# Performance work log

Hardware: AMD Instinct MI355X
Metric: run time of the kernel (lower is better)

Reference implementation:

```python
import jax, jax.numpy as jnp
import numpy as np

N_NODES = 50000
N_GRAPHS = 32
NODE_F = 16
GLOBAL_F = 2
HID = 300
LAT = 100
N_EDGES = 800000


def _glorot(key, shape):
    fan_in, fan_out = shape[0], shape[1]
    s = jnp.sqrt(2.0 / (fan_in + fan_out))
    return jax.random.normal(key, shape, dtype=jnp.float32) * s


def setup_inputs() -> dict:
    key = jax.random.key(0)
    ks = jax.random.split(key, 24)
    x = jax.random.normal(ks[0], (N_NODES, NODE_F), dtype=jnp.float32)
    edge_index = jax.random.randint(ks[1], (2, N_EDGES), 0, N_NODES, dtype=jnp.int64)
    batch = jnp.sort(jax.random.randint(ks[2], (N_NODES,), 0, N_GRAPHS, dtype=jnp.int64))
    u = jax.random.normal(ks[3], (N_GRAPHS, GLOBAL_F), dtype=jnp.float32)
    # layer 0: in=NODE_F, layer 1: in=LAT
    p = {}
    p['l0_w1'] = _glorot(ks[4], (2 * NODE_F, HID)); p['l0_b1'] = jnp.zeros((HID,), jnp.float32)
    p['l0_w2'] = _glorot(ks[5], (HID, HID));        p['l0_b2'] = jnp.zeros((HID,), jnp.float32)
    p['l0_w3'] = _glorot(ks[6], (HID, LAT));        p['l0_b3'] = jnp.zeros((LAT,), jnp.float32)
    p['l1_w1'] = _glorot(ks[7], (2 * LAT, HID));    p['l1_b1'] = jnp.zeros((HID,), jnp.float32)
    p['l1_w2'] = _glorot(ks[8], (HID, HID));        p['l1_b2'] = jnp.zeros((HID,), jnp.float32)
    p['l1_w3'] = _glorot(ks[9], (HID, LAT));        p['l1_b3'] = jnp.zeros((LAT,), jnp.float32)
    p['lin_w1'] = _glorot(ks[10], (LAT + GLOBAL_F, LAT)); p['lin_b1'] = jnp.zeros((LAT,), jnp.float32)
    p['lin_w2'] = _glorot(ks[11], (LAT, LAT));            p['lin_b2'] = jnp.zeros((LAT,), jnp.float32)
    p['lin_w3'] = _glorot(ks[12], (LAT, 1));              p['lin_b3'] = jnp.zeros((1,), jnp.float32)
    return dict(x=x, edge_index=edge_index, batch=batch, u=u, **p)


def _edge_layer(x, src, dst, w1, b1, w2, b2, w3, b3):
    # gather endpoints; torch_geometric default flow: x_j = x[src], x_i = x[dst]
    xi = x[dst]
    xj = x[src]
    inp = jnp.concatenate([xi, xj - xi], axis=-1)          # [E, 2*in]
    h = jax.nn.relu(inp @ w1 + b1)
    h = jax.nn.relu(h @ w2 + b2)
    m = h @ w3 + b3                                         # [E, out]
    s = jax.ops.segment_sum(m, dst, num_segments=N_NODES)  # scatter-sum to target nodes
    cnt = jax.ops.segment_sum(jnp.ones((m.shape[0],), m.dtype), dst, num_segments=N_NODES)
    return s / jnp.maximum(cnt, 1.0)[:, None]               # scatter-mean


def _mean_pool(x, batch):
    s = jax.ops.segment_sum(x, batch, num_segments=N_GRAPHS)
    cnt = jax.ops.segment_sum(jnp.ones((x.shape[0],), x.dtype), batch, num_segments=N_GRAPHS)
    return s / jnp.maximum(cnt, 1.0)[:, None]


def reference(x, edge_index, batch, u,
              l0_w1, l0_b1, l0_w2, l0_b2, l0_w3, l0_b3,
              l1_w1, l1_b1, l1_w2, l1_b2, l1_w3, l1_b3,
              lin_w1, lin_b1, lin_w2, lin_b2, lin_w3, lin_b3):
    src, dst = edge_index[0], edge_index[1]
    x = _edge_layer(x, src, dst, l0_w1, l0_b1, l0_w2, l0_b2, l0_w3, l0_b3)
    x = jax.nn.relu(x)
    x = _edge_layer(x, src, dst, l1_w1, l1_b1, l1_w2, l1_b2, l1_w3, l1_b3)
    x = jax.nn.relu(x)
    pooled = jnp.concatenate([_mean_pool(x, batch), u], axis=1)  # [G, LAT+GLOBAL_F]
    h = jax.nn.relu(pooled @ lin_w1 + lin_b1)
    h = jax.nn.relu(h @ lin_w2 + lin_b2)
    return h @ lin_w3 + lin_b3  # [G, 1]
```

## Files before the change

kernel.cpp:

```cpp
#include <hip/hip_runtime.h>
#include <cstdint>
#include <cstddef>

#define N_NODES  50000
#define N_GRAPHS 32
#define NODE_F   16
#define GLOBAL_F 2
#define HID      300
#define LAT      100
#define N_EDGES  800000

#define HIDP 320
#define LATP 128
#define NCT1 (HIDP/16)
#define NCT2 (LATP/16)
#define NKS  (HIDP/32)
#define EPB  96
#define NRT  6
#define ROWP 98
#define HSFS 132

typedef __bf16 bf16x8 __attribute__((ext_vector_type(8)));
typedef float  f32x4  __attribute__((ext_vector_type(4)));

__device__ __forceinline__ float relu_f(float x){ return fmaxf(x, 0.f); }

__device__ __forceinline__ unsigned short f2bf(float x){
  unsigned int u = __float_as_uint(x);
  u = (u + 0x7FFFu + ((u >> 16) & 1u)) >> 16;
  return (unsigned short)u;
}
__device__ __forceinline__ unsigned short f2bf_hw(float x){
  __bf16 h = (__bf16)x;
  return __builtin_bit_cast(unsigned short, h);
}
__device__ __forceinline__ float bf2f(unsigned int h){
  return __uint_as_float(h << 16);
}

__global__ void zero_kernel(float* __restrict__ p, int n){
  int i = blockIdx.x*blockDim.x + threadIdx.x;
  if (i < n) p[i] = 0.f;
}

__global__ void hist_kernel(const int* __restrict__ ei, int* __restrict__ hist){
  int e = blockIdx.x*blockDim.x + threadIdx.x;
  if (e < N_EDGES) atomicAdd(&hist[ei[N_EDGES + e]], 1);
}

__global__ __launch_bounds__(256) void scan_kernel(const int* __restrict__ hist,
                                                   int* __restrict__ woff){
  __shared__ int part[256];
  const int t = threadIdx.x;
  const int CH = (N_NODES + 255) / 256;
  const int lo = t*CH, hi = (lo + CH < N_NODES) ? lo + CH : N_NODES;
  int s = 0;
  for (int i = lo; i < hi; ++i) s += hist[i];
  part[t] = s;
  __syncthreads();
  for (int d = 1; d < 256; d <<= 1){
    int v = (t >= d) ? part[t-d] : 0;
    __syncthreads();
    part[t] += v;
    __syncthreads();
  }
  int run = (t == 0) ? 0 : part[t-1];
  for (int i = lo; i < hi; ++i){ woff[i] = run; run += hist[i]; }
}

__global__ void sort_kernel(const int* __restrict__ ei, int* __restrict__ woff,
                            int* __restrict__ es, int* __restrict__ ed){
  int e = blockIdx.x*blockDim.x + threadIdx.x;
  if (e < N_EDGES){
    int s = ei[e], d = ei[N_EDGES + e];
    int pos = atomicAdd(&woff[d], 1);
    es[pos] = s; ed[pos] = d;
  }
}

__global__ void gstart_kernel(const int* __restrict__ batch, int* __restrict__ gstart){
  int n = blockIdx.x*blockDim.x + threadIdx.x;
  if (n < N_NODES){
    int b = batch[n];
    if (n == 0){ for (int g = 0; g <= b; ++g) gstart[g] = 0; }
    else {
      int bp = batch[n-1];
      for (int g = bp+1; g <= b; ++g) gstart[g] = n;
    }
    if (n == N_NODES-1){ for (int g = b+1; g <= N_GRAPHS; ++g) gstart[g] = N_NODES; }
  }
}

__device__ __forceinline__ void pack_one(const float* __restrict__ w, int K, int N,
                                         int nct, unsigned short* __restrict__ out, int i){
  int j  = i & 7;
  int l  = (i >> 3) & 63;
  int t  = i >> 9;
  int ct = t % nct, ks = t / nct;
  int n = ct*16 + (l & 15);
  int k = ks*32 + ((l >> 4) << 3) + j;
  float v = (k < K && n < N) ? w[(size_t)k*N + n] : 0.f;
  out[i] = f2bf(v);
}

#define W2F_ELEMS (NKS*NCT1*512)
#define W3F_ELEMS (NKS*NCT2*512)

__global__ void pack_all(const float* __restrict__ w2a, const float* __restrict__ w3a,
                         const float* __restrict__ w2b, const float* __restrict__ w3b,
                         unsigned short* __restrict__ o2a, unsigned short* __restrict__ o3a,
                         unsigned short* __restrict__ o2b, unsigned short* __restrict__ o3b){
  int i = blockIdx.x*blockDim.x + threadIdx.x;
  if (i < W2F_ELEMS) pack_one(w2a, HID, HID, NCT1, o2a, i);
  else if (i < W2F_ELEMS + W3F_ELEMS) pack_one(w3a, HID, LAT, NCT2, o3a, i - W2F_ELEMS);
  else if (i < 2*W2F_ELEMS + W3F_ELEMS) pack_one(w2b, HID, HID, NCT1, o2b, i - W2F_ELEMS - W3F_ELEMS);
  else if (i < 2*W2F_ELEMS + 2*W3F_ELEMS) pack_one(w3b, HID, LAT, NCT2, o3b, i - 2*W2F_ELEMS - W3F_ELEMS);
}

template<int F>
__global__ void pack_w1frag(const float* __restrict__ w1,
                            unsigned short* __restrict__ out, int total){
  int i = blockIdx.x*blockDim.x + threadIdx.x;
  if (i >= total) return;
  int j  = i & 7;
  int l  = (i >> 3) & 63;
  int t  = i >> 9;
  int ct = t % 40, ks = t / 40;
  int n = ct*16 + (l & 15);
  int k = ks*32 + ((l >> 4) << 3) + j;
  float v = 0.f;
  if (k < F){
    if (n < HIDP){ if (n < HID) v = w1[(size_t)k*HID + n] - w1[(size_t)(F+k)*HID + n]; }
    else { int nn = n - HIDP; if (nn < HID) v = w1[(size_t)(F+k)*HID + nn]; }
  }
  out[i] = f2bf(v);
}

__global__ void pad_bias4(const float* __restrict__ a0, const float* __restrict__ a1,
                          const float* __restrict__ a2, const float* __restrict__ a3,
                          float* __restrict__ o0, float* __restrict__ o1,
                          float* __restrict__ o2, float* __restrict__ o3){
  int i = blockIdx.x*blockDim.x + threadIdx.x;
  if (i < HIDP){
    o0[i] = (i < HID) ? a0[i] : 0.f;
    o1[i] = (i < HID) ? a1[i] : 0.f;
    o2[i] = (i < HID) ? a2[i] : 0.f;
    o3[i] = (i < HID) ? a3[i] : 0.f;
  }
}

__global__ void cvt_x0(const float* __restrict__ x, unsigned short* __restrict__ xb){
  int i = blockIdx.x*blockDim.x + threadIdx.x;
  if (i < N_NODES*32){
    int n = i >> 5, c = i & 31;
    xb[i] = (c < NODE_F) ? f2bf(x[(size_t)n*NODE_F + c]) : 0;
  }
}

template<int KPAD>
__global__ __launch_bounds__(256) void node_gemm(
    const unsigned short* __restrict__ xb, const unsigned short* __restrict__ wf,
    unsigned short* __restrict__ Ub, unsigned short* __restrict__ Vb){
  constexpr int NCH = KPAD/8;
  __shared__ __align__(16) unsigned short at[NCH][66][8];
  const int tid = threadIdx.x;
  const int n0 = blockIdx.x*64;
  for (int i = tid; i < 64*NCH; i += 256){
    int row = i / NCH, c = i % NCH;
    int n = n0 + row; if (n >= N_NODES) n = N_NODES-1;
    *(uint4*)&at[c][row][0] = *(const uint4*)&xb[(size_t)n*KPAD + c*8];
  }
  __syncthreads();
  const int wave = tid >> 6, l = tid & 63;
  const int lrow = l & 15, lq = l >> 4;
  f32x4 acc[4][10];
  #pragma unroll
  for (int rt = 0; rt < 4; ++rt)
    #pragma unroll
    for (int c = 0; c < 10; ++c)
      acc[rt][c] = (f32x4){0.f,0.f,0.f,0.f};
  for (int ks = 0; ks < KPAD/32; ++ks){
    bf16x8 a[4];
    #pragma unroll
    for (int rt = 0; rt < 4; ++rt)
      a[rt] = __builtin_bit_cast(bf16x8, *(const uint4*)&at[4*ks + lq][16*rt + lrow][0]);
    #pragma unroll
    for (int c = 0; c < 10; ++c){
      int ct = wave*10 + c;
      bf16x8 b = __builtin_bit_cast(bf16x8,
                   *(const uint4*)&wf[(((size_t)(ks*40 + ct)) << 9) + l*8]);
      #pragma unroll
      for (int rt = 0; rt < 4; ++rt)
        acc[rt][c] = __builtin_amdgcn_mfma_f32_16x16x32_bf16(a[rt], b, acc[rt][c], 0, 0, 0);
    }
  }
  #pragma unroll
  for (int c = 0; c < 10; ++c){
    int col = (wave*10 + c)*16 + lrow;
    #pragma unroll
    for (int rt = 0; rt < 4; ++rt){
      #pragma unroll
      for (int r = 0; r < 4; ++r){
        int n = n0 + rt*16 + lq*4 + r;
        if (n < N_NODES){
          unsigned short hv = f2bf_hw(acc[rt][c][r]);
          if (col < HIDP) Ub[(size_t)n*HIDP + col] = hv;
          else            Vb[(size_t)n*HIDP + col - HIDP] = hv;
        }
      }
    }
  }
}

__global__ __launch_bounds__(256, 2) void edge_mfma(
    const int* __restrict__ es, const int* __restrict__ ed,
    const unsigned short* __restrict__ U, const unsigned short* __restrict__ V,
    const float* __restrict__ b1p, const unsigned short* __restrict__ w2f,
    const float* __restrict__ b2p, const unsigned short* __restrict__ w3f,
    float* __restrict__ nodeacc){
  __shared__ __align__(16) unsigned char smem[(HIDP/8)*ROWP*8*2];
  __shared__ int sdst[EPB];
  __shared__ int sflag[EPB];
  unsigned short* hsb = (unsigned short*)smem;
  float*          hsf = (float*)smem;
  #define HS(c,row) (hsb + (((c)*ROWP + (row)) << 3))

  const int tid = threadIdx.x;
  const int e0 = blockIdx.x * EPB;
  const int nvalid = (N_EDGES - e0 < EPB) ? (N_EDGES - e0) : EPB;
  if (tid < EPB) sdst[tid] = (tid < nvalid) ? ed[e0 + tid] : -1;

  #pragma unroll
  for (int it = 0; it < 15; ++it){
    int idx = tid + it*256;
    int e = idx / 40;
    int c = idx - e*40;
    int eg = e0 + e; if (eg >= N_EDGES) eg = N_EDGES - 1;
    const int dn = ed[eg], sn = es[eg];
    const uint4 uu = *(const uint4*)&U[(size_t)dn*HIDP + c*8];
    const uint4 vv = *(const uint4*)&V[(size_t)sn*HIDP + c*8];
    const float4 bl = *(const float4*)&b1p[c*8];
    const float4 bh = *(const float4*)&b1p[c*8 + 4];
    const unsigned int uarr[4] = {uu.x, uu.y, uu.z, uu.w};
    const unsigned int varr[4] = {vv.x, vv.y, vv.z, vv.w};
    const float barr[8] = {bl.x, bl.y, bl.z, bl.w, bh.x, bh.y, bh.z, bh.w};
    unsigned int ou[4];
    #pragma unroll
    for (int q = 0; q < 4; ++q){
      float f0 = relu_f(bf2f(uarr[q] & 0xFFFFu) + bf2f(varr[q] & 0xFFFFu) + barr[2*q]);
      float f1 = relu_f(bf2f(uarr[q] >> 16)     + bf2f(varr[q] >> 16)     + barr[2*q+1]);
      ou[q] = (unsigned int)f2bf_hw(f0) | ((unsigned int)f2bf_hw(f1) << 16);
    }
    *(uint4*)HS(c, e) = make_uint4(ou[0], ou[1], ou[2], ou[3]);
  }
  __syncthreads();

  const int wave = tid >> 6, l = tid & 63;
  const int lrow = l & 15, lq = l >> 4;

  f32x4 acc1[NRT][5];
  #pragma unroll
  for (int rt = 0; rt < NRT; ++rt)
    #pragma unroll
    for (int c = 0; c < 5; ++c)
      acc1[rt][c] = (f32x4){0.f,0.f,0.f,0.f};
  for (int ks = 0; ks < NKS; ++ks){
    bf16x8 a[NRT];
    #pragma unroll
    for (int rt = 0; rt < NRT; ++rt)
      a[rt] = __builtin_bit_cast(bf16x8, *(const uint4*)HS(4*ks + lq, 16*rt + lrow));
    #pragma unroll
    for (int c = 0; c < 5; ++c){
      int ct = wave*5 + c;
      bf16x8 b = __builtin_bit_cast(bf16x8,
                   *(const uint4*)&w2f[(((size_t)(ks*NCT1 + ct)) << 9) + l*8]);
      #pragma unroll
      for (int rt = 0; rt < NRT; ++rt)
        acc1[rt][c] = __builtin_amdgcn_mfma_f32_16x16x32_bf16(a[rt], b, acc1[rt][c], 0, 0, 0);
    }
  }
  __syncthreads();

  #pragma unroll
  for (int c = 0; c < 5; ++c){
    int col = (wave*5 + c)*16 + lrow;
    float b2v = b2p[col];
    #pragma unroll
    for (int rt = 0; rt < NRT; ++rt){
      #pragma unroll
      for (int r = 0; r < 4; ++r){
        int row = rt*16 + lq*4 + r;
        HS(col >> 3, row)[col & 7] = f2bf_hw(relu_f(acc1[rt][c][r] + b2v));
      }
    }
  }
  __syncthreads();

  f32x4 acc2[NRT][2];
  #pragma unroll
  for (int rt = 0; rt < NRT; ++rt)
    #pragma unroll
    for (int c = 0; c < 2; ++c)
      acc2[rt][c] = (f32x4){0.f,0.f,0.f,0.f};
  for (int ks = 0; ks < NKS; ++ks){
    bf16x8 a[NRT];
    #pragma unroll
    for (int rt = 0; rt < NRT; ++rt)
      a[rt] = __builtin_bit_cast(bf16x8, *(const uint4*)HS(4*ks + lq, 16*rt + lrow));
    #pragma unroll
    for (int c = 0; c < 2; ++c){
      int ct = wave*2 + c;
      bf16x8 b = __builtin_bit_cast(bf16x8,
                   *(const uint4*)&w3f[(((size_t)(ks*NCT2 + ct)) << 9) + l*8]);
      #pragma unroll
      for (int rt = 0; rt < NRT; ++rt)
        acc2[rt][c] = __builtin_amdgcn_mfma_f32_16x16x32_bf16(a[rt], b, acc2[rt][c], 0, 0, 0);
    }
  }
  __syncthreads();

  #pragma unroll
  for (int c = 0; c < 2; ++c){
    int col = (wave*2 + c)*16 + lrow;
    #pragma unroll
    for (int rt = 0; rt < NRT; ++rt){
      #pragma unroll
      for (int r = 0; r < 4; ++r){
        int row = rt*16 + lq*4 + r;
        hsf[row*HSFS + col] = acc2[rt][c][r];
      }
    }
  }
  if (tid < EPB) sflag[tid] = (tid == 0) || (sdst[tid] != sdst[tid-1]);
  __syncthreads();

  {
    const int col = tid & 127;
    if (col < LAT){
      for (int s = tid >> 7; s < EPB; s += 2){
        if (!sflag[s]) continue;
        int d = sdst[s];
        if (d < 0) continue;
        float sum = hsf[s*HSFS + col];
        int r = s + 1;
        while (r < EPB && !sflag[r]){ sum += hsf[r*HSFS + col]; ++r; }
        atomicAdd(&nodeacc[(size_t)d*LAT + col], sum);
      }
    }
  }
  #undef HS
}

__global__ void finalize_kernel(float* __restrict__ nodeacc, const int* __restrict__ hist,
                                const float* __restrict__ b3,
                                unsigned short* __restrict__ x1b){
  int idx = blockIdx.x*blockDim.x + threadIdx.x;
  if (idx < N_NODES*128){
    int n = idx >> 7, j = idx & 127;
    unsigned short o = 0;
    if (j < LAT){
      int c = hist[n];
      float v = nodeacc[(size_t)n*LAT + j] / fmaxf((float)c, 1.f);
      v += (c > 0) ? b3[j] : 0.f;
      o = f2bf_hw(relu_f(v));
      nodeacc[(size_t)n*LAT + j] = 0.f;
    }
    x1b[idx] = o;
  }
}

__global__ __launch_bounds__(512) void pool_seg(const unsigned short* __restrict__ x1b,
                                                const int* __restrict__ gstart,
                                                float* __restrict__ pooled){
  __shared__ float buf[3][128];
  const int g = blockIdx.x;
  const int lo = gstart[g], hi = gstart[g+1];
  const int col = threadIdx.x & 127, q = threadIdx.x >> 7;
  float s = 0.f;
  for (int n = lo + q; n < hi; n += 4) s += bf2f(x1b[(size_t)n*128 + col]);
  if (q) buf[q-1][col] = s;
  __syncthreads();
  if (q == 0 && col < LAT){
    float tot = s + buf[0][col] + buf[1][col] + buf[2][col];
    pooled[g*LAT + col] = tot / fmaxf((float)(hi - lo), 1.f);
  }
}

__global__ __launch_bounds__(128) void head_kernel(
    const float* __restrict__ pooled,
    const float* __restrict__ u,
    const float* __restrict__ w1, const float* __restrict__ bb1,
    const float* __restrict__ w2, const float* __restrict__ bb2,
    const float* __restrict__ w3, const float* __restrict__ bb3,
    float* __restrict__ out){
  __shared__ float p[N_GRAPHS][LAT+GLOBAL_F];
  __shared__ float h1[N_GRAPHS][LAT];
  __shared__ float h2[N_GRAPHS][LAT];
  const int tid = threadIdx.x;
  for (int t = tid; t < N_GRAPHS*LAT; t += 128){
    int g = t / LAT, k = t - g*LAT;
    p[g][k] = pooled[t];
  }
  for (int t = tid; t < N_GRAPHS*GLOBAL_F; t += 128){
    int g = t / GLOBAL_F, c = t - g*GLOBAL_F;
    p[g][LAT + c] = u[t];
  }
  __syncthreads();
  for (int t = tid; t < N_GRAPHS*LAT; t += 128){
    int g = t / LAT, j = t - g*LAT;
    float s = bb1[j];
    for (int k = 0; k < LAT+GLOBAL_F; k++) s += p[g][k]*w1[(size_t)k*LAT + j];
    h1[g][j] = relu_f(s);
  }
  __syncthreads();
  for (int t = tid; t < N_GRAPHS*LAT; t += 128){
    int g = t / LAT, j = t - g*LAT;
    float s = bb2[j];
    for (int k = 0; k < LAT; k++) s += h1[g][k]*w2[(size_t)k*LAT + j];
    h2[g][j] = relu_f(s);
  }
  __syncthreads();
  for (int t = tid; t < N_GRAPHS; t += 128){
    float s = bb3[0];
    for (int k = 0; k < LAT; k++) s += h2[t][k]*w3[k];
    out[t] = s;
  }
}

extern "C" void kernel_launch(void* const* d_in, const int* in_sizes, int n_in,
                              void* d_out, int out_size, void* d_ws, size_t ws_size,
                              hipStream_t stream){
  (void)in_sizes; (void)n_in; (void)out_size; (void)ws_size;
  const float* x     = (const float*)d_in[0];
  const int*   ei    = (const int*)d_in[1];
  const int*   batch = (const int*)d_in[2];
  const float* u     = (const float*)d_in[3];
  const float* l0_w1 = (const float*)d_in[4];  const float* l0_b1 = (const float*)d_in[5];
  const float* l0_w2 = (const float*)d_in[6];  const float* l0_b2 = (const float*)d_in[7];
  const float* l0_w3 = (const float*)d_in[8];  const float* l0_b3 = (const float*)d_in[9];
  const float* l1_w1 = (const float*)d_in[10]; const float* l1_b1 = (const float*)d_in[11];
  const float* l1_w2 = (const float*)d_in[12]; const float* l1_b2 = (const float*)d_in[13];
  const float* l1_w3 = (const float*)d_in[14]; const float* l1_b3 = (const float*)d_in[15];
  const float* lin_w1= (const float*)d_in[16]; const float* lin_b1= (const float*)d_in[17];
  const float* lin_w2= (const float*)d_in[18]; const float* lin_b2= (const float*)d_in[19];
  const float* lin_w3= (const float*)d_in[20]; const float* lin_b3= (const float*)d_in[21];

  char* wsb = (char*)d_ws;
  const size_t UV_BYTES  = (size_t)N_NODES*HIDP*sizeof(unsigned short);
  const size_t W1F0_ELEMS = (size_t)1*40*512;
  const size_t W1F1_ELEMS = (size_t)4*40*512;

  unsigned short* Ub   = (unsigned short*)wsb;  wsb += UV_BYTES;
  unsigned short* Vb   = (unsigned short*)wsb;  wsb += UV_BYTES;
  unsigned short* w2f0 = (unsigned short*)wsb;  wsb += (size_t)W2F_ELEMS*2;
  unsigned short* w3f0 = (unsigned short*)wsb;  wsb += (size_t)W3F_ELEMS*2;
  unsigned short* w2f1 = (unsigned short*)wsb;  wsb += (size_t)W2F_ELEMS*2;
  unsigned short* w3f1 = (unsigned short*)wsb;  wsb += (size_t)W3F_ELEMS*2;
  unsigned short* w1f0 = (unsigned short*)wsb;  wsb += W1F0_ELEMS*2;
  unsigned short* w1f1 = (unsigned short*)wsb;  wsb += W1F1_ELEMS*2;
  float* b1p0 = (float*)wsb;                    wsb += HIDP*4;
  float* b2p0 = (float*)wsb;                    wsb += HIDP*4;
  float* b1p1 = (float*)wsb;                    wsb += HIDP*4;
  float* b2p1 = (float*)wsb;                    wsb += HIDP*4;
  unsigned short* xb0 = (unsigned short*)wsb;   wsb += (size_t)N_NODES*32*2;
  unsigned short* x1b = (unsigned short*)wsb;   wsb += (size_t)N_NODES*128*2;
  float* nodeacc = (float*)wsb;                 wsb += (size_t)N_NODES*LAT*4;
  int*   hist    = (int*)wsb;                   wsb += (size_t)N_NODES*4;
  int*   woff    = (int*)wsb;                   wsb += (size_t)N_NODES*4;
  int*   es      = (int*)wsb;                   wsb += (size_t)N_EDGES*4;
  int*   ed      = (int*)wsb;                   wsb += (size_t)N_EDGES*4;
  int*   gstart  = (int*)wsb;                   wsb += 64*4;
  float* pooled  = (float*)wsb;                 wsb += (size_t)N_GRAPHS*LAT*4;

  {
    int zn = N_NODES*LAT + N_NODES;
    hipLaunchKernelGGL(zero_kernel, dim3((zn+255)/256), dim3(256), 0, stream, nodeacc, zn);
  }
  hipLaunchKernelGGL(hist_kernel, dim3((N_EDGES+255)/256), dim3(256), 0, stream, ei, hist);
  hipLaunchKernelGGL(scan_kernel, dim3(1), dim3(256), 0, stream, hist, woff);
  hipLaunchKernelGGL(sort_kernel, dim3((N_EDGES+255)/256), dim3(256), 0, stream,
                     ei, woff, es, ed);
  hipLaunchKernelGGL(gstart_kernel, dim3((N_NODES+255)/256), dim3(256), 0, stream,
                     batch, gstart);

  {
    int total = 2*W2F_ELEMS + 2*W3F_ELEMS;
    hipLaunchKernelGGL(pack_all, dim3((total+255)/256), dim3(256), 0, stream,
                       l0_w2, l0_w3, l1_w2, l1_w3, w2f0, w3f0, w2f1, w3f1);
  }
  hipLaunchKernelGGL(pack_w1frag<NODE_F>, dim3(((int)W1F0_ELEMS+255)/256), dim3(256), 0, stream,
                     l0_w1, w1f0, (int)W1F0_ELEMS);
  hipLaunchKernelGGL(pack_w1frag<LAT>, dim3(((int)W1F1_ELEMS+255)/256), dim3(256), 0, stream,
                     l1_w1, w1f1, (int)W1F1_ELEMS);
  hipLaunchKernelGGL(pad_bias4, dim3(2), dim3(256), 0, stream,
                     l0_b1, l0_b2, l1_b1, l1_b2, b1p0, b2p0, b1p1, b2p1);
  hipLaunchKernelGGL(cvt_x0, dim3((N_NODES*32+255)/256), dim3(256), 0, stream, x, xb0);

  const int NGB = (N_NODES + 63)/64;
  const int NEB = (N_EDGES + EPB - 1)/EPB;

  hipLaunchKernelGGL(node_gemm<32>, dim3(NGB), dim3(256), 0, stream, xb0, w1f0, Ub, Vb);
  hipLaunchKernelGGL(edge_mfma, dim3(NEB), dim3(256), 0, stream,
                     es, ed, Ub, Vb, b1p0, w2f0, b2p0, w3f0, nodeacc);
  hipLaunchKernelGGL(finalize_kernel, dim3((N_NODES*128+255)/256), dim3(256), 0, stream,
                     nodeacc, hist, l0_b3, x1b);

  hipLaunchKernelGGL(node_gemm<128>, dim3(NGB), dim3(256), 0, stream, x1b, w1f1, Ub, Vb);
  hipLaunchKernelGGL(edge_mfma, dim3(NEB), dim3(256), 0, stream,
                     es, ed, Ub, Vb, b1p1, w2f1, b2p1, w3f1, nodeacc);
  hipLaunchKernelGGL(finalize_kernel, dim3((N_NODES*128+255)/256), dim3(256), 0, stream,
                     nodeacc, hist, l1_b3, x1b);

  hipLaunchKernelGGL(pool_seg, dim3(N_GRAPHS), dim3(512), 0, stream, x1b, gstart, pooled);
  hipLaunchKernelGGL(head_kernel, dim3(1), dim3(128), 0, stream,
                     pooled, u, lin_w1, lin_b1, lin_w2, lin_b2, lin_w3, lin_b3,
                     (float*)d_out);
}
```

Baseline: 1.637 ms.

## Shrink edge tile to 64 for higher occupancy and merge prep kernels

Reduces edges per block from 96 to 64, which shrinks the MFMA accumulator arrays and shared tile so three blocks per CU fit instead of two. The gather is restructured so each lane owns one edge's src/dst indices instead of recomputing a division per element. Separately, the zero, pack, bias-pad and x-convert kernels are fused into one prep kernel, and gstart is folded into the sort kernel, cutting launch count. Tail handling is dropped because 800000 divides evenly by 64, which ties correctness to that edge count.

```diff
diff --git a/kernel.cpp b/kernel.cpp
--- a/kernel.cpp
+++ b/kernel.cpp
@@ -15,10 +15,14 @@
 #define NCT1 (HIDP/16)
 #define NCT2 (LATP/16)
 #define NKS  (HIDP/32)
-#define EPB  96
-#define NRT  6
-#define ROWP 98
+#define EPB  64
+#define ROWP 66
 #define HSFS 132
+
+#define W2F_ELEMS 102400
+#define W3F_ELEMS 40960
+#define W1F0_ELEMS 20480
+#define W1F1_ELEMS 81920
 
 typedef __bf16 bf16x8 __attribute__((ext_vector_type(8)));
 typedef float  f32x4  __attribute__((ext_vector_type(4)));
@@ -36,59 +40,6 @@
 }
 __device__ __forceinline__ float bf2f(unsigned int h){
   return __uint_as_float(h << 16);
-}
-
-__global__ void zero_kernel(float* __restrict__ p, int n){
-  int i = blockIdx.x*blockDim.x + threadIdx.x;
-  if (i < n) p[i] = 0.f;
-}
-
-__global__ void hist_kernel(const int* __restrict__ ei, int* __restrict__ hist){
-  int e = blockIdx.x*blockDim.x + threadIdx.x;
-  if (e < N_EDGES) atomicAdd(&hist[ei[N_EDGES + e]], 1);
-}
-
-__global__ __launch_bounds__(256) void scan_kernel(const int* __restrict__ hist,
-                                                   int* __restrict__ woff){
-  __shared__ int part[256];
-  const int t = threadIdx.x;
-  const int CH = (N_NODES + 255) / 256;
-  const int lo = t*CH, hi = (lo + CH < N_NODES) ? lo + CH : N_NODES;
-  int s = 0;
-  for (int i = lo; i < hi; ++i) s += hist[i];
-  part[t] = s;
-  __syncthreads();
-  for (int d = 1; d < 256; d <<= 1){
-    int v = (t >= d) ? part[t-d] : 0;
-    __syncthreads();
-    part[t] += v;
-    __syncthreads();
-  }
-  int run = (t == 0) ? 0 : part[t-1];
-  for (int i = lo; i < hi; ++i){ woff[i] = run; run += hist[i]; }
-}
-
-__global__ void sort_kernel(const int* __restrict__ ei, int* __restrict__ woff,
-                            int* __restrict__ es, int* __restrict__ ed){
-  int e = blockIdx.x*blockDim.x + threadIdx.x;
-  if (e < N_EDGES){
-    int s = ei[e], d = ei[N_EDGES + e];
-    int pos = atomicAdd(&woff[d], 1);
-    es[pos] = s; ed[pos] = d;
-  }
-}
-
-__global__ void gstart_kernel(const int* __restrict__ batch, int* __restrict__ gstart){
-  int n = blockIdx.x*blockDim.x + threadIdx.x;
-  if (n < N_NODES){
-    int b = batch[n];
-    if (n == 0){ for (int g = 0; g <= b; ++g) gstart[g] = 0; }
-    else {
-      int bp = batch[n-1];
-      for (int g = bp+1; g <= b; ++g) gstart[g] = n;
-    }
-    if (n == N_NODES-1){ for (int g = b+1; g <= N_GRAPHS; ++g) gstart[g] = N_NODES; }
-  }
 }
 
 __device__ __forceinline__ void pack_one(const float* __restrict__ w, int K, int N,
@@ -103,25 +54,8 @@
   out[i] = f2bf(v);
 }
 
-#define W2F_ELEMS (NKS*NCT1*512)
-#define W3F_ELEMS (NKS*NCT2*512)
-
-__global__ void pack_all(const float* __restrict__ w2a, const float* __restrict__ w3a,
-                         const float* __restrict__ w2b, const float* __restrict__ w3b,
-                         unsigned short* __restrict__ o2a, unsigned short* __restrict__ o3a,
-                         unsigned short* __restrict__ o2b, unsigned short* __restrict__ o3b){
-  int i = blockIdx.x*blockDim.x + threadIdx.x;
-  if (i < W2F_ELEMS) pack_one(w2a, HID, HID, NCT1, o2a, i);
-  else if (i < W2F_ELEMS + W3F_ELEMS) pack_one(w3a, HID, LAT, NCT2, o3a, i - W2F_ELEMS);
-  else if (i < 2*W2F_ELEMS + W3F_ELEMS) pack_one(w2b, HID, HID, NCT1, o2b, i - W2F_ELEMS - W3F_ELEMS);
-  else if (i < 2*W2F_ELEMS + 2*W3F_ELEMS) pack_one(w3b, HID, LAT, NCT2, o3b, i - 2*W2F_ELEMS - W3F_ELEMS);
-}
-
-template<int F>
-__global__ void pack_w1frag(const float* __restrict__ w1,
-                            unsigned short* __restrict__ out, int total){
-  int i = blockIdx.x*blockDim.x + threadIdx.x;
-  if (i >= total) return;
+__device__ __forceinline__ void pack_w1_one(const float* __restrict__ w1, int F,
+                                            unsigned short* __restrict__ out, int i){
   int j  = i & 7;
   int l  = (i >> 3) & 63;
   int t  = i >> 9;
@@ -136,24 +70,97 @@
   out[i] = f2bf(v);
 }
 
-__global__ void pad_bias4(const float* __restrict__ a0, const float* __restrict__ a1,
-                          const float* __restrict__ a2, const float* __restrict__ a3,
-                          float* __restrict__ o0, float* __restrict__ o1,
-                          float* __restrict__ o2, float* __restrict__ o3){
+#define PR_B0 (N_NODES*LAT + N_NODES)
+#define PR_B1 (PR_B0 + 2*W2F_ELEMS + 2*W3F_ELEMS)
+#define PR_B2 (PR_B1 + W1F0_ELEMS)
+#define PR_B3 (PR_B2 + W1F1_ELEMS)
+#define PR_B4 (PR_B3 + HIDP)
+#define PR_B5 (PR_B4 + N_NODES*32)
+
+__global__ void prep_kernel(
+    int* __restrict__ zero_region,
+    const float* __restrict__ w2a, const float* __restrict__ w3a,
+    const float* __restrict__ w2b, const float* __restrict__ w3b,
+    unsigned short* __restrict__ o2a, unsigned short* __restrict__ o3a,
+    unsigned short* __restrict__ o2b, unsigned short* __restrict__ o3b,
+    const float* __restrict__ w1a, unsigned short* __restrict__ o1a,
+    const float* __restrict__ w1b, unsigned short* __restrict__ o1b,
+    const float* __restrict__ ba0, const float* __restrict__ ba1,
+    const float* __restrict__ ba2, const float* __restrict__ ba3,
+    float* __restrict__ bo0, float* __restrict__ bo1,
+    float* __restrict__ bo2, float* __restrict__ bo3,
+    const float* __restrict__ x, unsigned short* __restrict__ xb){
   int i = blockIdx.x*blockDim.x + threadIdx.x;
-  if (i < HIDP){
-    o0[i] = (i < HID) ? a0[i] : 0.f;
-    o1[i] = (i < HID) ? a1[i] : 0.f;
-    o2[i] = (i < HID) ? a2[i] : 0.f;
-    o3[i] = (i < HID) ? a3[i] : 0.f;
-  }
-}
-
-__global__ void cvt_x0(const float* __restrict__ x, unsigned short* __restrict__ xb){
-  int i = blockIdx.x*blockDim.x + threadIdx.x;
-  if (i < N_NODES*32){
-    int n = i >> 5, c = i & 31;
-    xb[i] = (c < NODE_F) ? f2bf(x[(size_t)n*NODE_F + c]) : 0;
+  if (i < PR_B0){ zero_region[i] = 0; return; }
+  if (i < PR_B1){
+    int t = i - PR_B0;
+    if (t < W2F_ELEMS) pack_one(w2a, HID, HID, NCT1, o2a, t);
+    else if (t < W2F_ELEMS + W3F_ELEMS) pack_one(w3a, HID, LAT, NCT2, o3a, t - W2F_ELEMS);
+    else if (t < 2*W2F_ELEMS + W3F_ELEMS) pack_one(w2b, HID, HID, NCT1, o2b, t - W2F_ELEMS - W3F_ELEMS);
+    else pack_one(w3b, HID, LAT, NCT2, o3b, t - 2*W2F_ELEMS - W3F_ELEMS);
+    return;
+  }
+  if (i < PR_B2){ pack_w1_one(w1a, NODE_F, o1a, i - PR_B1); return; }
+  if (i < PR_B3){ pack_w1_one(w1b, LAT,    o1b, i - PR_B2); return; }
+  if (i < PR_B4){
+    int t = i - PR_B3;
+    bo0[t] = (t < HID) ? ba0[t] : 0.f;
+    bo1[t] = (t < HID) ? ba1[t] : 0.f;
+    bo2[t] = (t < HID) ? ba2[t] : 0.f;
+    bo3[t] = (t < HID) ? ba3[t] : 0.f;
+    return;
+  }
+  if (i < PR_B5){
+    int t = i - PR_B4;
+    int n = t >> 5, c = t & 31;
+    xb[t] = (c < NODE_F) ? f2bf(x[(size_t)n*NODE_F + c]) : 0;
+    return;
+  }
+}
+
+__global__ void hist_kernel(const int* __restrict__ ei, int* __restrict__ hist){
+  int e = blockIdx.x*blockDim.x + threadIdx.x;
+  if (e < N_EDGES) atomicAdd(&hist[ei[N_EDGES + e]], 1);
+}
+
+__global__ __launch_bounds__(256) void scan_kernel(const int* __restrict__ hist,
+                                                   int* __restrict__ woff){
+  __shared__ int part[256];
+  const int t = threadIdx.x;
+  const int CH = (N_NODES + 255) / 256;
+  const int lo = t*CH, hi = (lo + CH < N_NODES) ? lo + CH : N_NODES;
+  int s = 0;
+  for (int i = lo; i < hi; ++i) s += hist[i];
+  part[t] = s;
+  __syncthreads();
+  for (int d = 1; d < 256; d <<= 1){
+    int v = (t >= d) ? part[t-d] : 0;
+    __syncthreads();
+    part[t] += v;
+    __syncthreads();
+  }
+  int run = (t == 0) ? 0 : part[t-1];
+  for (int i = lo; i < hi; ++i){ woff[i] = run; run += hist[i]; }
+}
+
+__global__ void sort_gstart(const int* __restrict__ ei, int* __restrict__ woff,
+                            int* __restrict__ es, int* __restrict__ ed,
+                            const int* __restrict__ batch, int* __restrict__ gstart){
+  int e = blockIdx.x*blockDim.x + threadIdx.x;
+  if (e < N_EDGES){
+    int s = ei[e], d = ei[N_EDGES + e];
+    int pos = atomicAdd(&woff[d], 1);
+    es[pos] = s; ed[pos] = d;
+  }
+  if (e < N_NODES){
+    int n = e;
+    int b = batch[n];
+    if (n == 0){ for (int g = 0; g <= b; ++g) gstart[g] = 0; }
+    else {
+      int bp = batch[n-1];
+      for (int g = bp+1; g <= b; ++g) gstart[g] = n;
+    }
+    if (n == N_NODES-1){ for (int g = b+1; g <= N_GRAPHS; ++g) gstart[g] = N_NODES; }
   }
 }
 
@@ -212,7 +219,7 @@
   }
 }
 
-__global__ __launch_bounds__(256, 2) void edge_mfma(
+__global__ __launch_bounds__(256, 3) void edge_mfma(
     const int* __restrict__ es, const int* __restrict__ ed,
     const unsigned short* __restrict__ U, const unsigned short* __restrict__ V,
     const float* __restrict__ b1p, const unsigned short* __restrict__ w2f,
@@ -227,18 +234,18 @@
 
   const int tid = threadIdx.x;
   const int e0 = blockIdx.x * EPB;
-  const int nvalid = (N_EDGES - e0 < EPB) ? (N_EDGES - e0) : EPB;
-  if (tid < EPB) sdst[tid] = (tid < nvalid) ? ed[e0 + tid] : -1;
-
-  #pragma unroll
-  for (int it = 0; it < 15; ++it){
-    int idx = tid + it*256;
-    int e = idx / 40;
-    int c = idx - e*40;
-    int eg = e0 + e; if (eg >= N_EDGES) eg = N_EDGES - 1;
-    const int dn = ed[eg], sn = es[eg];
-    const uint4 uu = *(const uint4*)&U[(size_t)dn*HIDP + c*8];
-    const uint4 vv = *(const uint4*)&V[(size_t)sn*HIDP + c*8];
+  const int eL = tid & 63;
+  const int mysrc = es[e0 + eL];
+  const int mydst = ed[e0 + eL];
+  if (tid < EPB) sdst[tid] = mydst;
+
+  const size_t ubase = (size_t)mydst*HIDP;
+  const size_t vbase = (size_t)mysrc*HIDP;
+  #pragma unroll
+  for (int it = 0; it < 10; ++it){
+    int c = (tid + it*256) >> 6;
+    const uint4 uu = *(const uint4*)&U[ubase + c*8];
+    const uint4 vv = *(const uint4*)&V[vbase + c*8];
     const float4 bl = *(const float4*)&b1p[c*8];
     const float4 bh = *(const float4*)&b1p[c*8 + 4];
     const unsigned int uarr[4] = {uu.x, uu.y, uu.z, uu.w};
@@ -251,23 +258,23 @@
       float f1 = relu_f(bf2f(uarr[q] >> 16)     + bf2f(varr[q] >> 16)     + barr[2*q+1]);
       ou[q] = (unsigned int)f2bf_hw(f0) | ((unsigned int)f2bf_hw(f1) << 16);
     }
-    *(uint4*)HS(c, e) = make_uint4(ou[0], ou[1], ou[2], ou[3]);
+    *(uint4*)HS(c, eL) = make_uint4(ou[0], ou[1], ou[2], ou[3]);
   }
   __syncthreads();
 
   const int wave = tid >> 6, l = tid & 63;
   const int lrow = l & 15, lq = l >> 4;
 
-  f32x4 acc1[NRT][5];
-  #pragma unroll
-  for (int rt = 0; rt < NRT; ++rt)
+  f32x4 acc1[4][5];
+  #pragma unroll
+  for (int rt = 0; rt < 4; ++rt)
     #pragma unroll
     for (int c = 0; c < 5; ++c)
       acc1[rt][c] = (f32x4){0.f,0.f,0.f,0.f};
   for (int ks = 0; ks < NKS; ++ks){
-    bf16x8 a[NRT];
-    #pragma unroll
-    for (int rt = 0; rt < NRT; ++rt)
+    bf16x8 a[4];
+    #pragma unroll
+    for (int rt = 0; rt < 4; ++rt)
       a[rt] = __builtin_bit_cast(bf16x8, *(const uint4*)HS(4*ks + lq, 16*rt + lrow));
     #pragma unroll
     for (int c = 0; c < 5; ++c){
@@ -275,7 +282,7 @@
       bf16x8 b = __builtin_bit_cast(bf16x8,
                    *(const uint4*)&w2f[(((size_t)(ks*NCT1 + ct)) << 9) + l*8]);
       #pragma unroll
-      for (int rt = 0; rt < NRT; ++rt)
+      for (int rt = 0; rt < 4; ++rt)
         acc1[rt][c] = __builtin_amdgcn_mfma_f32_16x16x32_bf16(a[rt], b, acc1[rt][c], 0, 0, 0);
     }
   }
@@ -286,7 +293,7 @@
     int col = (wave*5 + c)*16 + lrow;
     float b2v = b2p[col];
     #pragma unroll
-    for (int rt = 0; rt < NRT; ++rt){
+    for (int rt = 0; rt < 4; ++rt){
       #pragma unroll
       for (int r = 0; r < 4; ++r){
         int row = rt*16 + lq*4 + r;
@@ -296,16 +303,16 @@
   }
   __syncthreads();
 
-  f32x4 acc2[NRT][2];
-  #pragma unroll
-  for (int rt = 0; rt < NRT; ++rt)
+  f32x4 acc2[4][2];
+  #pragma unroll
+  for (int rt = 0; rt < 4; ++rt)
     #pragma unroll
     for (int c = 0; c < 2; ++c)
       acc2[rt][c] = (f32x4){0.f,0.f,0.f,0.f};
   for (int ks = 0; ks < NKS; ++ks){
-    bf16x8 a[NRT];
-    #pragma unroll
-    for (int rt = 0; rt < NRT; ++rt)
+    bf16x8 a[4];
+    #pragma unroll
+    for (int rt = 0; rt < 4; ++rt)
       a[rt] = __builtin_bit_cast(bf16x8, *(const uint4*)HS(4*ks + lq, 16*rt + lrow));
     #pragma unroll
     for (int c = 0; c < 2; ++c){
@@ -313,7 +320,7 @@
       bf16x8 b = __builtin_bit_cast(bf16x8,
                    *(const uint4*)&w3f[(((size_t)(ks*NCT2 + ct)) << 9) + l*8]);
       #pragma unroll
-      for (int rt = 0; rt < NRT; ++rt)
+      for (int rt = 0; rt < 4; ++rt)
         acc2[rt][c] = __builtin_amdgcn_mfma_f32_16x16x32_bf16(a[rt], b, acc2[rt][c], 0, 0, 0);
     }
   }
@@ -323,7 +330,7 @@
   for (int c = 0; c < 2; ++c){
     int col = (wave*2 + c)*16 + lrow;
     #pragma unroll
-    for (int rt = 0; rt < NRT; ++rt){
+    for (int rt = 0; rt < 4; ++rt){
       #pragma unroll
       for (int r = 0; r < 4; ++r){
         int row = rt*16 + lq*4 + r;
@@ -340,7 +347,6 @@
       for (int s = tid >> 7; s < EPB; s += 2){
         if (!sflag[s]) continue;
         int d = sdst[s];
-        if (d < 0) continue;
         float sum = hsf[s*HSFS + col];
         int r = s + 1;
         while (r < EPB && !sflag[r]){ sum += hsf[r*HSFS + col]; ++r; }
@@ -446,9 +452,7 @@
   const float* lin_w3= (const float*)d_in[20]; const float* lin_b3= (const float*)d_in[21];
 
   char* wsb = (char*)d_ws;
-  const size_t UV_BYTES  = (size_t)N_NODES*HIDP*sizeof(unsigned short);
-  const size_t W1F0_ELEMS = (size_t)1*40*512;
-  const size_t W1F1_ELEMS = (size_t)4*40*512;
+  const size_t UV_BYTES = (size_t)N_NODES*HIDP*sizeof(unsigned short);
 
   unsigned short* Ub   = (unsigned short*)wsb;  wsb += UV_BYTES;
   unsigned short* Vb   = (unsigned short*)wsb;  wsb += UV_BYTES;
@@ -456,8 +460,8 @@
   unsigned short* w3f0 = (unsigned short*)wsb;  wsb += (size_t)W3F_ELEMS*2;
   unsigned short* w2f1 = (unsigned short*)wsb;  wsb += (size_t)W2F_ELEMS*2;
   unsigned short* w3f1 = (unsigned short*)wsb;  wsb += (size_t)W3F_ELEMS*2;
-  unsigned short* w1f0 = (unsigned short*)wsb;  wsb += W1F0_ELEMS*2;
-  unsigned short* w1f1 = (unsigned short*)wsb;  wsb += W1F1_ELEMS*2;
+  unsigned short* w1f0 = (unsigned short*)wsb;  wsb += (size_t)W1F0_ELEMS*2;
+  unsigned short* w1f1 = (unsigned short*)wsb;  wsb += (size_t)W1F1_ELEMS*2;
   float* b1p0 = (float*)wsb;                    wsb += HIDP*4;
   float* b2p0 = (float*)wsb;                    wsb += HIDP*4;
   float* b1p1 = (float*)wsb;                    wsb += HIDP*4;
@@ -472,32 +476,19 @@
   int*   gstart  = (int*)wsb;                   wsb += 64*4;
   float* pooled  = (float*)wsb;                 wsb += (size_t)N_GRAPHS*LAT*4;
 
-  {
-    int zn = N_NODES*LAT + N_NODES;
-    hipLaunchKernelGGL(zero_kernel, dim3((zn+255)/256), dim3(256), 0, stream, nodeacc, zn);
-  }
+  hipLaunchKernelGGL(prep_kernel, dim3((PR_B5+255)/256), dim3(256), 0, stream,
+                     (int*)nodeacc,
+                     l0_w2, l0_w3, l1_w2, l1_w3, w2f0, w3f0, w2f1, w3f1,
+                     l0_w1, w1f0, l1_w1, w1f1,
+                     l0_b1, l0_b2, l1_b1, l1_b2, b1p0, b2p0, b1p1, b2p1,
+                     x, xb0);
   hipLaunchKernelGGL(hist_kernel, dim3((N_EDGES+255)/256), dim3(256), 0, stream, ei, hist);
   hipLaunchKernelGGL(scan_kernel, dim3(1), dim3(256), 0, stream, hist, woff);
-  hipLaunchKernelGGL(sort_kernel, dim3((N_EDGES+255)/256), dim3(256), 0, stream,
-                     ei, woff, es, ed);
-  hipLaunchKernelGGL(gstart_kernel, dim3((N_NODES+255)/256), dim3(256), 0, stream,
-                     batch, gstart);
-
-  {
-    int total = 2*W2F_ELEMS + 2*W3F_ELEMS;
-    hipLaunchKernelGGL(pack_all, dim3((total+255)/256), dim3(256), 0, stream,
-                       l0_w2, l0_w3, l1_w2, l1_w3, w2f0, w3f0, w2f1, w3f1);
-  }
-  hipLaunchKernelGGL(pack_w1frag<NODE_F>, dim3(((int)W1F0_ELEMS+255)/256), dim3(256), 0, stream,
-                     l0_w1, w1f0, (int)W1F0_ELEMS);
-  hipLaunchKernelGGL(pack_w1frag<LAT>, dim3(((int)W1F1_ELEMS+255)/256), dim3(256), 0, stream,
-                     l1_w1, w1f1, (int)W1F1_ELEMS);
-  hipLaunchKernelGGL(pad_bias4, dim3(2), dim3(256), 0, stream,
-                     l0_b1, l0_b2, l1_b1, l1_b2, b1p0, b2p0, b1p1, b2p1);
-  hipLaunchKernelGGL(cvt_x0, dim3((N_NODES*32+255)/256), dim3(256), 0, stream, x, xb0);
+  hipLaunchKernelGGL(sort_gstart, dim3((N_EDGES+255)/256), dim3(256), 0, stream,
+                     ei, woff, es, ed, batch, gstart);
 
   const int NGB = (N_NODES + 63)/64;
-  const int NEB = (N_EDGES + EPB - 1)/EPB;
+  const int NEB = N_EDGES/EPB;
 
   hipLaunchKernelGGL(node_gemm<32>, dim3(NGB), dim3(256), 0, stream, xb0, w1f0, Ub, Vb);
   hipLaunchKernelGGL(edge_mfma, dim3(NEB), dim3(256), 0, stream,
```

New measurement: 1.495 ms. -8.7%, faster.
